# Kernel tuning notes

Hardware: AMD Instinct MI355X
Metric: run time of the kernel (lower is better)

## Reference

```python
import jax, jax.numpy as jnp
import numpy as np

K = 3          # kernel size
STRIDE = 1
PAD = 1
DIL = 1
K2 = K * K     # number of sampling locations per output pixel


def conv2d(x, w, b, stride=STRIDE, pad=PAD, dil=DIL):
    # x: [B,C,H,W], w: [O,I,K,K], b: [O]
    out = jax.lax.conv_general_dilated(
        x, w, window_strides=(stride, stride),
        padding=[(pad, pad), (pad, pad)], rhs_dilation=(dil, dil),
        dimension_numbers=('NCHW', 'OIHW', 'NCHW'))
    return out + b[None, :, None, None]


def bilinear_sample(x, sy, sx):
    # x: [B,C,H,W]; sy, sx: [B,K2,Ho,Wo] float sampling coords (y, x)
    # zero padding outside the image (torchvision deform_conv2d semantics)
    B, C, H, W = x.shape
    x_flat = x.reshape(B, C, H * W)

    y0 = jnp.floor(sy)
    x0 = jnp.floor(sx)
    wy1 = sy - y0  # frac weights
    wx1 = sx - x0
    wy0 = 1.0 - wy1
    wx0 = 1.0 - wx1

    def gather(yi, xi):
        valid = ((yi >= 0) & (yi < H) & (xi >= 0) & (xi < W)).astype(x.dtype)
        yc = jnp.clip(yi, 0, H - 1).astype(jnp.int32)
        xc = jnp.clip(xi, 0, W - 1).astype(jnp.int32)
        idx = (yc * W + xc).reshape(B, 1, -1)  # [B,1,K2*Ho*Wo]
        v = jnp.take_along_axis(x_flat, idx, axis=2)  # [B,C,K2*Ho*Wo]
        v = v.reshape(B, C, *yi.shape[1:])            # [B,C,K2,Ho,Wo]
        return v * valid[:, None]

    out = (gather(y0,     x0    ) * (wy0 * wx0)[:, None]
         + gather(y0,     x0 + 1) * (wy0 * wx1)[:, None]
         + gather(y0 + 1, x0    ) * (wy1 * wx0)[:, None]
         + gather(y0 + 1, x0 + 1) * (wy1 * wx1)[:, None])
    return out  # [B,C,K2,Ho,Wo]


def setup_inputs() -> dict:
    key = jax.random.key(0)
    ks = jax.random.split(key, 6)
    B, C, H, W = 4, 64, 128, 128
    Cout = 64
    x = jax.random.normal(ks[0], (B, C, H, W), jnp.float32)
    # offset conv: 2*K2 output channels; small init -> small offsets (realistic)
    w_off = jax.random.normal(ks[1], (2 * K2, C, K, K), jnp.float32) * 0.01
    b_off = jnp.zeros((2 * K2,), jnp.float32)
    # mask conv: K2 output channels, sigmoid activation
    w_mask = jax.random.normal(ks[2], (K2, C, K, K), jnp.float32) * 0.01
    b_mask = jnp.zeros((K2,), jnp.float32)  # mask_init_bias = 0
    # main deformable conv weights
    w = jax.random.normal(ks[3], (Cout, C, K, K), jnp.float32) * (1.0 / np.sqrt(C * K2))
    b = jnp.zeros((Cout,), jnp.float32)
    return {"x": x, "w_off": w_off, "b_off": b_off,
            "w_mask": w_mask, "b_mask": b_mask, "w": w, "b": b}


def reference(x, w_off, b_off, w_mask, b_mask, w, b):
    B, C, H, W = x.shape
    Cout = w.shape[0]

    offset = conv2d(x, w_off, b_off)                    # [B,2*K2,Ho,Wo]
    mask = jax.nn.sigmoid(conv2d(x, w_mask, b_mask))    # [B,K2,Ho,Wo]
    Ho, Wo = offset.shape[2], offset.shape[3]

    off = offset.reshape(B, K2, 2, Ho, Wo)
    dy, dx = off[:, :, 0], off[:, :, 1]                 # torchvision layout: (y,x) pairs

    ki = (jnp.arange(K2) // K).astype(jnp.float32)      # kernel row index
    kj = (jnp.arange(K2) % K).astype(jnp.float32)       # kernel col index
    base_y = (jnp.arange(Ho, dtype=jnp.float32) * STRIDE - PAD)[None, :, None] \
             + (ki * DIL)[:, None, None]                # [K2,Ho,1]
    base_x = (jnp.arange(Wo, dtype=jnp.float32) * STRIDE - PAD)[None, None, :] \
             + (kj * DIL)[:, None, None]                # [K2,1,Wo]

    sy = base_y[None] + dy                              # [B,K2,Ho,Wo]
    sx = base_x[None] + dx

    sampled = bilinear_sample(x, sy, sx) * mask[:, None]  # [B,C,K2,Ho,Wo]
    out = jnp.einsum('bckhw,ock->bohw', sampled, w.reshape(Cout, C, K2))
    return out + b[None, :, None, None]
```

## Files before the change

### kernel.cpp

```cpp
#include <hip/hip_runtime.h>
#include <math.h>

typedef __attribute__((ext_vector_type(8))) short short8;
typedef __attribute__((ext_vector_type(4))) float f32x4;
typedef unsigned short ushort_t;
typedef unsigned int uint_t;

#define HH 128
#define WW 128
#define CC 64
#define HWp 16384

__device__ inline ushort_t f2bf(float f) {
    uint_t u = __float_as_uint(f);
    uint_t r = (u + 0x7FFFu + ((u >> 16) & 1u)) >> 16;
    return (ushort_t)r;
}
__device__ inline float blo(uint_t u) { return __uint_as_float(u << 16); }
__device__ inline float bhi(uint_t u) { return __uint_as_float(u & 0xFFFF0000u); }
__device__ inline short8 bc8(uint4 v) { return __builtin_bit_cast(short8, v); }

__global__ __launch_bounds__(256) void k_pack(const float* __restrict__ w_off,
        const float* __restrict__ w_mask, const float* __restrict__ w,
        ushort_t* __restrict__ wpom, ushort_t* __restrict__ wpm) {
    int idx = blockIdx.x * 256 + threadIdx.x;
    if (idx < 18432) {
        int e = idx;
        int j = e & 7, l = (e >> 3) & 63, mf = (e >> 9) & 1, ks = e >> 10;
        int ch = mf * 16 + (l & 15);
        int k = ks * 32 + ((l >> 4) << 3) + j;
        int c = k & 63, kk = k >> 6;
        float v = 0.f;
        if (ch < 18) v = w_off[(ch * CC + c) * 9 + kk];
        else if (ch < 27) v = w_mask[((ch - 18) * CC + c) * 9 + kk];
        wpom[idx] = f2bf(v);
    } else if (idx < 18432 + 36864) {
        int e = idx - 18432;
        int j = e & 7, l = (e >> 3) & 63, mf = (e >> 9) & 3, ks = e >> 11;
        int o = mf * 16 + (l & 15);
        int k = ks * 32 + ((l >> 4) << 3) + j;
        int c = k & 63, kk = k >> 6;
        wpm[e] = f2bf(w[(o * CC + c) * 9 + kk]);
    }
}

__global__ __launch_bounds__(256) void k_transpose_x(const float* __restrict__ x,
                                                     ushort_t* __restrict__ xtb) {
    __shared__ float tile[64][65];
    int bid = blockIdx.x;
    int xs = (bid & 1) * 64;
    int y  = (bid >> 1) & 127;
    int b  = bid >> 8;
    int t = threadIdx.x, lane = t & 63, g = t >> 6;
#pragma unroll
    for (int i = 0; i < 16; ++i) {
        int c = i * 4 + g;
        tile[c][lane] = x[(((size_t)b * CC + c) * HH + y) * WW + xs + lane];
    }
    __syncthreads();
#pragma unroll
    for (int i = 0; i < 16; ++i) {
        int xx = i * 4 + g;
        xtb[(((size_t)b * HH + y) * WW + xs + xx) * CC + lane] = f2bf(tile[lane][xx]);
    }
}

__global__ __launch_bounds__(512, 4) void k_conv_om(const ushort_t* __restrict__ xtb,
        const uint4* __restrict__ wpom, const float* __restrict__ b_off,
        const float* __restrict__ b_mask, float* __restrict__ om) {
    __shared__ ushort_t xrow[3 * 132 * 64];
    int blk = blockIdx.x;
    int y = blk & 127, b = blk >> 7;
    int t = threadIdx.x;

    for (int ky = 0; ky < 3; ++ky) {
        int yy = y + ky - 1;
        bool ok = (yy >= 0) && (yy < HH);
#pragma unroll
        for (int i = 0; i < 2; ++i) {
            int t2 = i * 512 + t;
            int colr = t2 >> 3;
            int c0 = (t2 & 7) * 8;
            uint4 v = make_uint4(0u, 0u, 0u, 0u);
            if (ok) v = *(const uint4*)&xtb[(((size_t)b * HWp) + yy * WW + colr) * CC + c0];
            int col = colr + 1;
            int idx = ((ky * 132 + col) * 64 + c0) ^ ((col & 7) << 3);
            *(uint4*)&xrow[idx] = v;
        }
    }
    if (t < 48) {
        int ky = t >> 4, cs = (t >> 3) & 1, chn = t & 7;
        int col = cs ? 129 : 0;
        int idx = ((ky * 132 + col) * 64 + chn * 8) ^ ((col & 7) << 3);
        *(uint4*)&xrow[idx] = make_uint4(0u, 0u, 0u, 0u);
    }
    __syncthreads();

    int lane = t & 63, w = t >> 6;
    int lm = lane & 15, lg = lane >> 4;
    int px = w * 16 + lm;
    f32x4 acc[2] = {};
#pragma unroll
    for (int ks = 0; ks < 18; ++ks) {
        int kk = ks >> 1;
        int kyy = kk / 3, kxx = kk % 3;
        int c0 = (ks & 1) * 32 + lg * 8;
        short8 a0 = bc8(wpom[(ks * 2 + 0) * 64 + lane]);
        short8 a1 = bc8(wpom[(ks * 2 + 1) * 64 + lane]);
        int col = px + kxx;
        int idx = ((kyy * 132 + col) * 64 + c0) ^ ((col & 7) << 3);
        short8 bf = *(const short8*)&xrow[idx];
        acc[0] = __builtin_amdgcn_mfma_f32_16x16x32_bf16(a0, bf, acc[0], 0, 0, 0);
        acc[1] = __builtin_amdgcn_mfma_f32_16x16x32_bf16(a1, bf, acc[1], 0, 0, 0);
    }
#pragma unroll
    for (int mf = 0; mf < 2; ++mf)
#pragma unroll
        for (int r = 0; r < 4; ++r) {
            int ch = mf * 16 + lg * 4 + r;
            if (ch < 27) {
                float v = acc[mf][r] + (ch < 18 ? b_off[ch] : b_mask[ch - 18]);
                if (ch >= 18) v = 1.f / (1.f + __expf(-v));
                om[(((size_t)b * 27 + ch) << 14) + (y << 7) + px] = v;
            }
        }
}

__global__ __launch_bounds__(512, 4) void k_fused(const ushort_t* __restrict__ xtb,
        const float* __restrict__ om, const uint4* __restrict__ wpm,
        const float* __restrict__ bias, float* __restrict__ out) {
    __shared__ __align__(16) ushort_t sm[32 * 576];
    __shared__ __align__(16) float prm[288 * 8];
    int blk = blockIdx.x;
    int b = blk >> 9, rem = blk & 511;
    int y = rem >> 2, xs = (rem & 3) * 32;
    int t = threadIdx.x, lane = t & 63, w = t >> 6;
    const char* xbB = (const char*)xtb + ((size_t)b << 21);
    const float* omb = om + (((size_t)b * 27) << 14) + (y << 7) + xs;

    if (t < 288) {
        int k = t >> 5, px = t & 31;
        int ki = k / 3, kj = k - ki * 3;
        int x = xs + px;
        float dy = omb[((2 * k) << 14) + px];
        float dx = omb[((2 * k + 1) << 14) + px];
        float m  = omb[((18 + k) << 14) + px];
        float sy = (float)(y - 1 + ki) + dy;
        float sx = (float)(x - 1 + kj) + dx;
        float fy = floorf(sy), fx = floorf(sx);
        float wy1 = sy - fy, wx1 = sx - fx;
        float wy0 = 1.f - wy1, wx0 = 1.f - wx1;
        int iy0 = (int)fy, ix0 = (int)fx;
        int iy1 = iy0 + 1, ix1 = ix0 + 1;
        bool vy0 = (iy0 >= 0) & (iy0 < HH);
        bool vy1 = (iy1 >= 0) & (iy1 < HH);
        float wyr0 = vy0 ? wy0 : (vy1 ? wy1 : 0.f);
        int   ry0  = vy0 ? iy0 : (vy1 ? iy1 : 0);
        float wyr1 = (vy0 & vy1) ? wy1 : 0.f;
        int   ry1  = min(max(iy1, 0), HH - 1);
        int bx = min(max(ix0, 0), WW - 2);
        float wxh0 = (bx == ix0) ? wx0 : ((bx == ix1) ? wx1 : 0.f);
        float wxh1 = (bx + 1 == ix1) ? wx1 : ((bx + 1 == ix0) ? wx0 : 0.f);
        int s = px * 9 + k;
        float* pp = prm + s * 8;
        pp[0] = m * wyr0 * wxh0;
        pp[1] = m * wyr0 * wxh1;
        pp[2] = m * wyr1 * wxh0;
        pp[3] = m * wyr1 * wxh1;
        pp[4] = __uint_as_float((uint_t)(((ry0 << 7) + bx) << 7));
        pp[5] = __uint_as_float((uint_t)(((ry1 << 7) + bx) << 7));
        pp[6] = __uint_as_float((uint_t)(px * 576 + k * 64));
        pp[7] = __uint_as_float((uint_t)(((px ^ k) & 7) << 3));
    }
    __syncthreads();

    {
        int g = lane & 15;
        int q = lane >> 4;
        int sbase = w * 36 + q;
        int g8 = g << 3;
#pragma unroll
        for (int i = 0; i < 9; ++i) {
            int s = sbase + i * 4;
            const float* pp = prm + s * 8;
            f32x4 wv  = *(const f32x4*)pp;
            f32x4 aux = *(const f32x4*)(pp + 4);
            uint_t aT = __float_as_uint(aux.x) + (uint_t)g8;
            uint_t aB = __float_as_uint(aux.y) + (uint_t)g8;
            uint2 tl = *(const uint2*)(xbB + aT);
            uint2 tr = *(const uint2*)(xbB + aT + 128);
            uint2 bl = *(const uint2*)(xbB + aB);
            uint2 br = *(const uint2*)(xbB + aB + 128);
            float s0 = wv.x*blo(tl.x) + wv.y*blo(tr.x) + wv.z*blo(bl.x) + wv.w*blo(br.x);
            float s1 = wv.x*bhi(tl.x) + wv.y*bhi(tr.x) + wv.z*bhi(bl.x) + wv.w*bhi(br.x);
            float s2 = wv.x*blo(tl.y) + wv.y*blo(tr.y) + wv.z*blo(bl.y) + wv.w*blo(br.y);
            float s3 = wv.x*bhi(tl.y) + wv.y*bhi(tr.y) + wv.z*bhi(bl.y) + wv.w*bhi(br.y);
            uint_t r01, r23;
            asm("v_cvt_pk_bf16_f32 %0, %1, %2" : "=v"(r01) : "v"(s0), "v"(s1));
            asm("v_cvt_pk_bf16_f32 %0, %1, %2" : "=v"(r23) : "v"(s2), "v"(s3));
            int widx = (int)((__float_as_uint(aux.z) + (uint_t)(g << 2)) ^ __float_as_uint(aux.w));
            *(uint2*)&sm[widx] = make_uint2(r01, r23);
        }
    }
    __syncthreads();

    int lm = lane & 15, lg = lane >> 4;
    int mf = w & 3, nh = w >> 2;
    int px_r = (nh << 4) + lm;
    f32x4 acc = {};
#pragma unroll
    for (int ks = 0; ks < 18; ++ks) {
        short8 af = bc8(wpm[((ks << 2) + mf) * 64 + lane]);
        int bidx = (px_r * 576 + (ks << 5) + (lg << 3)) ^ (((px_r ^ (ks >> 1)) & 7) << 3);
        short8 bf = *(const short8*)&sm[bidx];
        acc = __builtin_amdgcn_mfma_f32_16x16x32_bf16(af, bf, acc, 0, 0, 0);
    }
#pragma unroll
    for (int r = 0; r < 4; ++r) {
        int o = (mf << 4) + (lg << 2) + r;
        out[(((size_t)b * 64 + o) << 14) + (y << 7) + xs + px_r] = acc[r] + bias[o];
    }
}

extern "C" void kernel_launch(void* const* d_in, const int* in_sizes, int n_in,
                              void* d_out, int out_size, void* d_ws, size_t ws_size,
                              hipStream_t stream) {
    const float* x      = (const float*)d_in[0];
    const float* w_off  = (const float*)d_in[1];
    const float* b_off  = (const float*)d_in[2];
    const float* w_mask = (const float*)d_in[3];
    const float* b_mask = (const float*)d_in[4];
    const float* w      = (const float*)d_in[5];
    const float* bias   = (const float*)d_in[6];
    float* out = (float*)d_out;

    char* ws = (char*)d_ws;
    ushort_t* xtb  = (ushort_t*)(ws);
    float*    om   = (float*)(ws + 8388608);
    ushort_t* wpom = (ushort_t*)(ws + 15466496);
    ushort_t* wpm  = (ushort_t*)(ws + 15503360);

    hipLaunchKernelGGL(k_pack, dim3(216), dim3(256), 0, stream,
                       w_off, w_mask, w, wpom, wpm);
    hipLaunchKernelGGL(k_transpose_x, dim3(1024), dim3(256), 0, stream, x, xtb);
    hipLaunchKernelGGL(k_conv_om, dim3(512), dim3(512), 0, stream,
                       xtb, (const uint4*)wpom, b_off, b_mask, om);
    hipLaunchKernelGGL(k_fused, dim3(2048), dim3(512), 0, stream,
                       xtb, om, (const uint4*)wpm, bias, out);
}
```

Measured before the change: 59.27 us.

## Feed bilinear samples straight into MFMA registers, one row per block

The fused deformable kernel no longer writes bilinear-interpolated samples to a shared-memory im2col tile. Each lane now gathers 16-byte vectors and builds the MFMA B operand directly in registers, and each wave computes all 64 output channels for 16 pixels. Blocks now cover a full 128-pixel row, so the grid shrinks from 2048 to 512 blocks and the per-pixel parameter table is larger. This removes the LDS round trip and one barrier, but it cuts the number of blocks and may raise register pressure and scatter more of the weight loads across lanes.

After: 70.37 us. +18.7%, slower.

```diff
diff --git a/kernel.cpp b/kernel.cpp
--- a/kernel.cpp
+++ b/kernel.cpp
@@ -19,6 +19,22 @@
 __device__ inline float blo(uint_t u) { return __uint_as_float(u << 16); }
 __device__ inline float bhi(uint_t u) { return __uint_as_float(u & 0xFFFF0000u); }
 __device__ inline short8 bc8(uint4 v) { return __builtin_bit_cast(short8, v); }
+
+__device__ inline uint_t pk2(f32x4 wv, uint_t a, uint_t b, uint_t c, uint_t d) {
+    float lo = wv.x * blo(a) + wv.y * blo(b) + wv.z * blo(c) + wv.w * blo(d);
+    float hi = wv.x * bhi(a) + wv.y * bhi(b) + wv.z * bhi(c) + wv.w * bhi(d);
+    uint_t r;
+    asm("v_cvt_pk_bf16_f32 %0, %1, %2" : "=v"(r) : "v"(lo), "v"(hi));
+    return r;
+}
+__device__ inline short8 bilerp8(f32x4 wv, uint4 A, uint4 B, uint4 C, uint4 D) {
+    uint4 r;
+    r.x = pk2(wv, A.x, B.x, C.x, D.x);
+    r.y = pk2(wv, A.y, B.y, C.y, D.y);
+    r.z = pk2(wv, A.z, B.z, C.z, D.z);
+    r.w = pk2(wv, A.w, B.w, C.w, D.w);
+    return __builtin_bit_cast(short8, r);
+}
 
 __global__ __launch_bounds__(256) void k_pack(const float* __restrict__ w_off,
         const float* __restrict__ w_mask, const float* __restrict__ w,
@@ -129,24 +145,21 @@
 __global__ __launch_bounds__(512, 4) void k_fused(const ushort_t* __restrict__ xtb,
         const float* __restrict__ om, const uint4* __restrict__ wpm,
         const float* __restrict__ bias, float* __restrict__ out) {
-    __shared__ __align__(16) ushort_t sm[32 * 576];
-    __shared__ __align__(16) float prm[288 * 8];
+    __shared__ __align__(16) float prm[1152 * 8];
     int blk = blockIdx.x;
-    int b = blk >> 9, rem = blk & 511;
-    int y = rem >> 2, xs = (rem & 3) * 32;
+    int b = blk >> 7, y = blk & 127;
     int t = threadIdx.x, lane = t & 63, w = t >> 6;
     const char* xbB = (const char*)xtb + ((size_t)b << 21);
-    const float* omb = om + (((size_t)b * 27) << 14) + (y << 7) + xs;
-
-    if (t < 288) {
-        int k = t >> 5, px = t & 31;
+    const float* omb = om + (((size_t)b * 27) << 14) + (y << 7);
+
+    for (int s = t; s < 1152; s += 512) {
+        int k = s >> 7, px = s & 127;
         int ki = k / 3, kj = k - ki * 3;
-        int x = xs + px;
         float dy = omb[((2 * k) << 14) + px];
         float dx = omb[((2 * k + 1) << 14) + px];
         float m  = omb[((18 + k) << 14) + px];
         float sy = (float)(y - 1 + ki) + dy;
-        float sx = (float)(x - 1 + kj) + dx;
+        float sx = (float)(px - 1 + kj) + dx;
         float fy = floorf(sy), fx = floorf(sx);
         float wy1 = sy - fy, wx1 = sx - fx;
         float wy0 = 1.f - wy1, wx0 = 1.f - wx1;
@@ -161,64 +174,55 @@
         int bx = min(max(ix0, 0), WW - 2);
         float wxh0 = (bx == ix0) ? wx0 : ((bx == ix1) ? wx1 : 0.f);
         float wxh1 = (bx + 1 == ix1) ? wx1 : ((bx + 1 == ix0) ? wx0 : 0.f);
-        int s = px * 9 + k;
-        float* pp = prm + s * 8;
+        float* pp = prm + (px * 9 + k) * 8;
         pp[0] = m * wyr0 * wxh0;
         pp[1] = m * wyr0 * wxh1;
         pp[2] = m * wyr1 * wxh0;
         pp[3] = m * wyr1 * wxh1;
         pp[4] = __uint_as_float((uint_t)(((ry0 << 7) + bx) << 7));
         pp[5] = __uint_as_float((uint_t)(((ry1 << 7) + bx) << 7));
-        pp[6] = __uint_as_float((uint_t)(px * 576 + k * 64));
-        pp[7] = __uint_as_float((uint_t)(((px ^ k) & 7) << 3));
     }
     __syncthreads();
 
-    {
-        int g = lane & 15;
-        int q = lane >> 4;
-        int sbase = w * 36 + q;
-        int g8 = g << 3;
-#pragma unroll
-        for (int i = 0; i < 9; ++i) {
-            int s = sbase + i * 4;
-            const float* pp = prm + s * 8;
-            f32x4 wv  = *(const f32x4*)pp;
-            f32x4 aux = *(const f32x4*)(pp + 4);
-            uint_t aT = __float_as_uint(aux.x) + (uint_t)g8;
-            uint_t aB = __float_as_uint(aux.y) + (uint_t)g8;
-            uint2 tl = *(const uint2*)(xbB + aT);
-            uint2 tr = *(const uint2*)(xbB + aT + 128);
-            uint2 bl = *(const uint2*)(xbB + aB);
-            uint2 br = *(const uint2*)(xbB + aB + 128);
-            float s0 = wv.x*blo(tl.x) + wv.y*blo(tr.x) + wv.z*blo(bl.x) + wv.w*blo(br.x);
-            float s1 = wv.x*bhi(tl.x) + wv.y*bhi(tr.x) + wv.z*bhi(bl.x) + wv.w*bhi(br.x);
-            float s2 = wv.x*blo(tl.y) + wv.y*blo(tr.y) + wv.z*blo(bl.y) + wv.w*blo(br.y);
-            float s3 = wv.x*bhi(tl.y) + wv.y*bhi(tr.y) + wv.z*bhi(bl.y) + wv.w*bhi(br.y);
-            uint_t r01, r23;
-            asm("v_cvt_pk_bf16_f32 %0, %1, %2" : "=v"(r01) : "v"(s0), "v"(s1));
-            asm("v_cvt_pk_bf16_f32 %0, %1, %2" : "=v"(r23) : "v"(s2), "v"(s3));
-            int widx = (int)((__float_as_uint(aux.z) + (uint_t)(g << 2)) ^ __float_as_uint(aux.w));
-            *(uint2*)&sm[widx] = make_uint2(r01, r23);
-        }
-    }
-    __syncthreads();
-
-    int lm = lane & 15, lg = lane >> 4;
-    int mf = w & 3, nh = w >> 2;
-    int px_r = (nh << 4) + lm;
-    f32x4 acc = {};
-#pragma unroll
-    for (int ks = 0; ks < 18; ++ks) {
-        short8 af = bc8(wpm[((ks << 2) + mf) * 64 + lane]);
-        int bidx = (px_r * 576 + (ks << 5) + (lg << 3)) ^ (((px_r ^ (ks >> 1)) & 7) << 3);
-        short8 bf = *(const short8*)&sm[bidx];
-        acc = __builtin_amdgcn_mfma_f32_16x16x32_bf16(af, bf, acc, 0, 0, 0);
-    }
+    int lm = lane & 15, cq = lane >> 4;
+    int px = (w << 4) + lm;
+    uint_t cqb = (uint_t)(cq << 4);
+    f32x4 acc0 = {}, acc1 = {}, acc2 = {}, acc3 = {};
+#pragma unroll
+    for (int k = 0; k < 9; ++k) {
+        const float* pp = prm + (px * 9 + k) * 8;
+        f32x4 wv = *(const f32x4*)pp;
+        uint_t aT = __float_as_uint(pp[4]) + cqb;
+        uint_t aB = __float_as_uint(pp[5]) + cqb;
+        uint4 tl0 = *(const uint4*)(xbB + aT);
+        uint4 tr0 = *(const uint4*)(xbB + aT + 128);
+        uint4 bl0 = *(const uint4*)(xbB + aB);
+        uint4 br0 = *(const uint4*)(xbB + aB + 128);
+        uint4 tl1 = *(const uint4*)(xbB + aT + 64);
+        uint4 tr1 = *(const uint4*)(xbB + aT + 192);
+        uint4 bl1 = *(const uint4*)(xbB + aB + 64);
+        uint4 br1 = *(const uint4*)(xbB + aB + 192);
+        short8 bf0 = bilerp8(wv, tl0, tr0, bl0, br0);
+        short8 bf1 = bilerp8(wv, tl1, tr1, bl1, br1);
+        int ka = (k << 3) * 64 + lane;
+        acc0 = __builtin_amdgcn_mfma_f32_16x16x32_bf16(bc8(wpm[ka +   0]), bf0, acc0, 0, 0, 0);
+        acc1 = __builtin_amdgcn_mfma_f32_16x16x32_bf16(bc8(wpm[ka +  64]), bf0, acc1, 0, 0, 0);
+        acc2 = __builtin_amdgcn_mfma_f32_16x16x32_bf16(bc8(wpm[ka + 128]), bf0, acc2, 0, 0, 0);
+        acc3 = __builtin_amdgcn_mfma_f32_16x16x32_bf16(bc8(wpm[ka + 192]), bf0, acc3, 0, 0, 0);
+        acc0 = __builtin_amdgcn_mfma_f32_16x16x32_bf16(bc8(wpm[ka + 256]), bf1, acc0, 0, 0, 0);
+        acc1 = __builtin_amdgcn_mfma_f32_16x16x32_bf16(bc8(wpm[ka + 320]), bf1, acc1, 0, 0, 0);
+        acc2 = __builtin_amdgcn_mfma_f32_16x16x32_bf16(bc8(wpm[ka + 384]), bf1, acc2, 0, 0, 0);
+        acc3 = __builtin_amdgcn_mfma_f32_16x16x32_bf16(bc8(wpm[ka + 448]), bf1, acc3, 0, 0, 0);
+    }
+
+    size_t obase = ((size_t)b << 20) + (y << 7) + px;
 #pragma unroll
     for (int r = 0; r < 4; ++r) {
-        int o = (mf << 4) + (lg << 2) + r;
-        out[(((size_t)b * 64 + o) << 14) + (y << 7) + xs + px_r] = acc[r] + bias[o];
+        int o0 = cq * 4 + r;
+        out[obase + (size_t)(o0     ) * HWp] = acc0[r] + bias[o0];
+        out[obase + (size_t)(o0 + 16) * HWp] = acc1[r] + bias[o0 + 16];
+        out[obase + (size_t)(o0 + 32) * HWp] = acc2[r] + bias[o0 + 32];
+        out[obase + (size_t)(o0 + 48) * HWp] = acc3[r] + bias[o0 + 48];
     }
 }
 
@@ -245,6 +249,6 @@
     hipLaunchKernelGGL(k_transpose_x, dim3(1024), dim3(256), 0, stream, x, xtb);
     hipLaunchKernelGGL(k_conv_om, dim3(512), dim3(512), 0, stream,
                        xtb, (const uint4*)wpom, b_off, b_mask, om);
-    hipLaunchKernelGGL(k_fused, dim3(2048), dim3(512), 0, stream,
+    hipLaunchKernelGGL(k_fused, dim3(512), dim3(512), 0, stream,
                        xtb, om, (const uint4*)wpm, bias, out);
 }
```
